# Optimization experiments

Measured on AMD Instinct MI355X. Metric: run time of the kernel, lower is better.

Reference implementation:

```python
import jax, jax.numpy as jnp
import numpy as np

SCALE = 1.0 / (64 ** 0.5)  # 1/sqrt(dim_key)

def setup_inputs() -> dict:
    key = jax.random.key(0)
    ks = jax.random.split(key, 8)
    B, S, D, H, dk = 4, 2048, 1024, 16, 64
    s = 0.02
    return {
        "values": jax.random.normal(ks[0], (B, S, D), jnp.float32),
        "queries": jax.random.normal(ks[1], (B, S, D), jnp.float32),
        "keys": jax.random.normal(ks[2], (B, S, D), jnp.float32),
        "Wq": jax.random.normal(ks[3], (H, D, dk), jnp.float32) * s,
        "bq": jnp.zeros((H, dk), jnp.float32),
        "Wk": jax.random.normal(ks[4], (H, D, dk), jnp.float32) * s,
        "bk": jnp.zeros((H, dk), jnp.float32),
        "Wv": jax.random.normal(ks[5], (H, D, dk), jnp.float32) * s,
        "bv": jnp.zeros((H, dk), jnp.float32),
        "Wo": jax.random.normal(ks[6], (D, D), jnp.float32) * s,
        "bo": jnp.zeros((D,), jnp.float32),
    }

def reference(values, queries, keys, Wq, bq, Wk, bk, Wv, bv, Wo, bo):
    # Per-head projections, batched across heads: [B,S,D] x [H,D,dk] -> [B,H,S,dk]
    q = jnp.einsum('bsd,hdk->bhsk', queries, Wq) + bq[None, :, None, :]
    k = jnp.einsum('bsd,hdk->bhsk', keys, Wk) + bk[None, :, None, :]
    v = jnp.einsum('bsd,hdk->bhsk', values, Wv) + bv[None, :, None, :]
    # Scaled dot-product scores [B,H,S,S]
    scores = jnp.einsum('bhqk,bhsk->bhqs', q, k) * SCALE
    S = scores.shape[-1]
    causal = jnp.tril(jnp.ones((S, S), bool))
    scores = jnp.where(causal, scores, jnp.float32(-1e19))
    attn = jax.nn.softmax(scores, axis=-1)
    ctx = jnp.einsum('bhqs,bhsk->bhqk', attn, v)  # [B,H,S,dk]
    # Concat heads along last axis (head-major, matching tf.concat order)
    B, H, Sq, dk = ctx.shape
    ctx = jnp.transpose(ctx, (0, 2, 1, 3)).reshape(B, Sq, H * dk)
    return ctx @ Wo + bo
```

## Files before the change

### kernel.cpp

```cpp
#include <hip/hip_runtime.h>
#include <hip/hip_bf16.h>
#include <cstdint>

#define B_ 4
#define H_ 16
#define S_ 2048
#define D_ 1024
#define DK 64
#define QSCALE 0.18033688f

typedef float f32x4 __attribute__((ext_vector_type(4)));
typedef short bf8 __attribute__((ext_vector_type(8)));
typedef unsigned short u16;

__device__ __forceinline__ u16 f2bf(float x){
  union { float f; uint32_t u; } c; c.f = x;
  uint32_t u = c.u;
  uint32_t r = (u + 0x7FFFu + ((u >> 16) & 1u)) >> 16;
  return (u16)r;
}

__device__ __forceinline__ uint32_t pk2bf(float a, float b){
  __hip_bfloat162 t = __float22bfloat162_rn(make_float2(a, b));
  uint32_t r; __builtin_memcpy(&r, &t, 4); return r;
}

__device__ __forceinline__ void gl16(const void* g, void* l){
  __builtin_amdgcn_global_load_lds(
      (const __attribute__((address_space(1))) void*)g,
      (__attribute__((address_space(3))) void*)l, 16, 0, 0);
}

__global__ __launch_bounds__(256) void cvt_in(
    const float* __restrict__ q, const float* __restrict__ k,
    const float* __restrict__ v, u16* __restrict__ o)
{
  const size_t N8 = (size_t)1 << 20;
  const size_t tot = 3 * N8;
  const size_t step = (size_t)gridDim.x * 256;
  for (size_t g0 = (size_t)blockIdx.x*256 + threadIdx.x; g0 < tot; g0 += step){
    int t = (int)(g0 >> 20);
    size_t r = g0 & (N8 - 1);
    const float* src = (t==0 ? q : (t==1 ? k : v));
    const float4* s4 = reinterpret_cast<const float4*>(src + r*8);
    float4 a = s4[0], b = s4[1];
    uint4 w;
    w.x = pk2bf(a.x,a.y); w.y = pk2bf(a.z,a.w);
    w.z = pk2bf(b.x,b.y); w.w = pk2bf(b.z,b.w);
    *reinterpret_cast<uint4*>(o + ((size_t)t << 23) + r*8) = w;
  }
}

__global__ __launch_bounds__(256) void wtrans3(
    const float* __restrict__ Wq, const float* __restrict__ Wk,
    const float* __restrict__ Wv, u16* __restrict__ oq,
    u16* __restrict__ ok, u16* __restrict__ ov)
{
  __shared__ u16 T[64*72];
  const int tid = threadIdx.x;
  const int z = blockIdx.z, t = z >> 4, hh = z & 15;
  const float* src = (t==0 ? Wq : t==1 ? Wk : Wv) + (size_t)hh * (D_*DK);
  u16* dst = (t==0 ? oq : t==1 ? ok : ov) + (size_t)hh * (DK*D_);
  const int r0 = blockIdx.y*64;
  #pragma unroll
  for (int p=0;p<4;++p){
    int r  = p*16 + (tid>>4);
    int c4 = (tid&15)*4;
    float4 v = *reinterpret_cast<const float4*>(&src[(size_t)(r0+r)*DK + c4]);
    uint2 w; w.x = pk2bf(v.x, v.y); w.y = pk2bf(v.z, v.w);
    *reinterpret_cast<uint2*>(&T[r*72 + c4]) = w;
  }
  __syncthreads();
  const int c = tid>>2, rg = (tid&3)*16;
  u16 tmp[16];
  #pragma unroll
  for (int i=0;i<16;++i) tmp[i] = T[(rg+i)*72 + c];
  *reinterpret_cast<bf8*>(&dst[(size_t)c*D_ + r0 + rg])     = *reinterpret_cast<bf8*>(&tmp[0]);
  *reinterpret_cast<bf8*>(&dst[(size_t)c*D_ + r0 + rg + 8]) = *reinterpret_cast<bf8*>(&tmp[8]);
}

__global__ __launch_bounds__(256) void wtrans(
    const float* __restrict__ in, u16* __restrict__ out, int R, int C)
{
  __shared__ u16 T[64*72];
  const int tid = threadIdx.x;
  const int r0 = blockIdx.y*64, c0 = blockIdx.x*64;
  #pragma unroll
  for (int p=0;p<4;++p){
    int r  = p*16 + (tid>>4);
    int c4 = (tid&15)*4;
    float4 v = *reinterpret_cast<const float4*>(&in[(size_t)(r0+r)*C + c0 + c4]);
    uint2 w; w.x = pk2bf(v.x, v.y); w.y = pk2bf(v.z, v.w);
    *reinterpret_cast<uint2*>(&T[r*72 + c4]) = w;
  }
  __syncthreads();
  const int c = tid>>2, rg = (tid&3)*16;
  u16 tmp[16];
  #pragma unroll
  for (int i=0;i<16;++i) tmp[i] = T[(rg+i)*72 + c];
  *reinterpret_cast<bf8*>(&out[(size_t)(c0+c)*R + r0 + rg])     = *reinterpret_cast<bf8*>(&tmp[0]);
  *reinterpret_cast<bf8*>(&out[(size_t)(c0+c)*R + r0 + rg + 8]) = *reinterpret_cast<bf8*>(&tmp[8]);
}

__global__ __launch_bounds__(256) void gemm_qkv(
    const u16* __restrict__ Ab,
    const u16* __restrict__ Bq, const u16* __restrict__ Bk,
    const u16* __restrict__ Bv,
    const float* __restrict__ bq, const float* __restrict__ bk,
    const float* __restrict__ bv,
    u16* __restrict__ oq, u16* __restrict__ ok, u16* __restrict__ ov)
{
  __shared__ u16 As[2][128*64];
  __shared__ u16 Bs[2][128*64];
  const int tid = threadIdx.x;
  const int wid = tid>>6, lane = tid&63, g = lane>>4, l15 = lane&15;
  const int z = blockIdx.x >> 9, bid = blockIdx.x & 511;
  const u16* A     = Ab + ((size_t)z << 23);
  const u16*   Bt  = (z==0 ? Bq : z==1 ? Bk : Bv);
  const float* bias= (z==0 ? bq : z==1 ? bk : bv);
  u16* Out         = (z==0 ? oq : z==1 ? ok : ov);
  const float osc  = (z==0 ? QSCALE : 1.0f);
  const int xcd = bid & 7, i = bid >> 3;
  const int cb = i & 7, rb = xcd*8 + (i>>3);
  const int row0 = rb*128, col0 = cb*128;
  const int wr = wid>>1, wc = wid&1;

  f32x4 acc[4][4];
  #pragma unroll
  for (int m=0;m<4;++m)
    #pragma unroll
    for (int n=0;n<4;++n) acc[m][n] = (f32x4){0.f,0.f,0.f,0.f};

  auto STAGE = [&](int buf, int k0){
    #pragma unroll
    for (int p=0;p<4;++p){
      int r0l = wid*32 + p*8;
      int row = r0l + (lane>>3);
      int ch = (lane&7) ^ (row&7);
      gl16(A  + (size_t)(row0+row)*D_ + k0 + ch*8, &As[buf][r0l*64]);
      gl16(Bt + (size_t)(col0+row)*D_ + k0 + ch*8, &Bs[buf][r0l*64]);
    }
  };

  int cur = 0;
  STAGE(0, 0);
  asm volatile("s_waitcnt vmcnt(0)" ::: "memory");
  __syncthreads();

  for (int k0 = 0; k0 < D_; k0 += 64) {
    if (k0 + 64 < D_) STAGE(cur^1, k0 + 64);

    bf8 af[4][2], bfm[4][2];
    #pragma unroll
    for (int m=0;m<4;++m){
      int row = wr*64 + m*16 + l15;
      af[m][0] = *reinterpret_cast<const bf8*>(&As[cur][row*64 + ((g     ^(row&7))*8)]);
      af[m][1] = *reinterpret_cast<const bf8*>(&As[cur][row*64 + (((4+g) ^(row&7))*8)]);
    }
    #pragma unroll
    for (int n=0;n<4;++n){
      int row = wc*64 + n*16 + l15;
      bfm[n][0] = *reinterpret_cast<const bf8*>(&Bs[cur][row*64 + ((g     ^(row&7))*8)]);
      bfm[n][1] = *reinterpret_cast<const bf8*>(&Bs[cur][row*64 + (((4+g) ^(row&7))*8)]);
    }
    #pragma unroll
    for (int m=0;m<4;++m)
      #pragma unroll
      for (int n=0;n<4;++n){
        acc[m][n] = __builtin_amdgcn_mfma_f32_16x16x32_bf16(af[m][0], bfm[n][0], acc[m][n], 0,0,0);
        acc[m][n] = __builtin_amdgcn_mfma_f32_16x16x32_bf16(af[m][1], bfm[n][1], acc[m][n], 0,0,0);
      }
    asm volatile("s_waitcnt vmcnt(0)" ::: "memory");
    __syncthreads();
    cur ^= 1;
  }

  #pragma unroll
  for (int m=0;m<4;++m){
    #pragma unroll
    for (int n=0;n<4;++n){
      int col = col0 + wc*64 + n*16 + l15;
      float bs = bias[col];
      if (z == 2){
        int rowb = row0 + wr*64 + m*16 + g*4;
        int b = rowb>>11, s = rowb&2047;
        int h = col>>6, dkk = col&63;
        ushort4 pk;
        pk.x = f2bf(acc[m][n][0]+bs); pk.y = f2bf(acc[m][n][1]+bs);
        pk.z = f2bf(acc[m][n][2]+bs); pk.w = f2bf(acc[m][n][3]+bs);
        *reinterpret_cast<ushort4*>(&Out[(((size_t)(b*H_+h)*DK)+dkk)*S_ + s]) = pk;
      } else {
        #pragma unroll
        for (int r=0;r<4;++r){
          int row = row0 + wr*64 + m*16 + g*4 + r;
          float v = (acc[m][n][r] + bs)*osc;
          int b = row>>11, s = row&2047;
          int h = col>>6, dkk = col&63;
          Out[(((size_t)(b*H_+h)*S_)+s)*DK + dkk] = f2bf(v);
        }
      }
    }
  }
}

__global__ __launch_bounds__(256) void gemm_out(
    const u16* __restrict__ A, const u16* __restrict__ Bt,
    const float* __restrict__ bias, float* __restrict__ Outp)
{
  __shared__ u16 As[2][128*64];
  __shared__ u16 Bs[2][128*64];
  const int tid = threadIdx.x;
  const int wid = tid>>6, lane = tid&63, g = lane>>4, l15 = lane&15;
  const int bid = blockIdx.x;
  const int xcd = bid & 7, i = bid >> 3;
  const int cb = i & 7, rb = xcd*8 + (i>>3);
  const int row0 = rb*128, col0 = cb*128;
  const int wr = wid>>1, wc = wid&1;

  f32x4 acc[4][4];
  #pragma unroll
  for (int m=0;m<4;++m)
    #pragma unroll
    for (int n=0;n<4;++n) acc[m][n] = (f32x4){0.f,0.f,0.f,0.f};

  auto STAGE = [&](int buf, int k0){
    #pragma unroll
    for (int p=0;p<4;++p){
      int r0l = wid*32 + p*8;
      int row = r0l + (lane>>3);
      int ch = (lane&7) ^ (row&7);
      gl16(A  + (size_t)(row0+row)*D_ + k0 + ch*8, &As[buf][r0l*64]);
      gl16(Bt + (size_t)(col0+row)*D_ + k0 + ch*8, &Bs[buf][r0l*64]);
    }
  };

  int cur = 0;
  STAGE(0, 0);
  asm volatile("s_waitcnt vmcnt(0)" ::: "memory");
  __syncthreads();

  for (int k0 = 0; k0 < D_; k0 += 64) {
    if (k0 + 64 < D_) STAGE(cur^1, k0 + 64);

    bf8 af[4][2], bfm[4][2];
    #pragma unroll
    for (int m=0;m<4;++m){
      int row = wr*64 + m*16 + l15;
      af[m][0] = *reinterpret_cast<const bf8*>(&As[cur][row*64 + ((g     ^(row&7))*8)]);
      af[m][1] = *reinterpret_cast<const bf8*>(&As[cur][row*64 + (((4+g) ^(row&7))*8)]);
    }
    #pragma unroll
    for (int n=0;n<4;++n){
      int row = wc*64 + n*16 + l15;
      bfm[n][0] = *reinterpret_cast<const bf8*>(&Bs[cur][row*64 + ((g     ^(row&7))*8)]);
      bfm[n][1] = *reinterpret_cast<const bf8*>(&Bs[cur][row*64 + (((4+g) ^(row&7))*8)]);
    }
    #pragma unroll
    for (int m=0;m<4;++m)
      #pragma unroll
      for (int n=0;n<4;++n){
        acc[m][n] = __builtin_amdgcn_mfma_f32_16x16x32_bf16(af[m][0], bfm[n][0], acc[m][n], 0,0,0);
        acc[m][n] = __builtin_amdgcn_mfma_f32_16x16x32_bf16(af[m][1], bfm[n][1], acc[m][n], 0,0,0);
      }
    asm volatile("s_waitcnt vmcnt(0)" ::: "memory");
    __syncthreads();
    cur ^= 1;
  }

  #pragma unroll
  for (int m=0;m<4;++m){
    #pragma unroll
    for (int n=0;n<4;++n){
      int col = col0 + wc*64 + n*16 + l15;
      float bs = bias[col];
      #pragma unroll
      for (int r=0;r<4;++r){
        int row = row0 + wr*64 + m*16 + g*4 + r;
        Outp[(size_t)row*D_ + col] = acc[m][n][r] + bs;
      }
    }
  }
}

__global__ __launch_bounds__(256) void attn_kernel(
    const u16* __restrict__ qp, const u16* __restrict__ kp,
    const u16* __restrict__ vt, u16* __restrict__ ctx)
{
  __shared__ u16 Kl[2][64*64];
  __shared__ u16 Vl[2][64*64];
  __shared__ u16 Pl[4][32*72];
  const int tid = threadIdx.x;
  const int wid = tid>>6, lane = tid&63, g = lane>>4, l15 = lane&15;
  const int bid0 = blockIdx.x;
  const int xx = bid0 & 7, yy = bid0 >> 3;
  const int bh = xx + 8*(yy >> 3);
  const int jj = yy & 7;
  const int b = bh >> 4, h = bh & 15;
  const size_t base = (size_t)bh * S_ * DK;

  bf8 ones;
  #pragma unroll
  for (int i=0;i<8;++i) ones[i] = (short)0x3F80;

  const int qts[2] = { jj, 15-jj };

  #pragma unroll 1
  for (int qi=0; qi<2; ++qi){
    const int qt = qts[qi];
    const int Q0 = qt*128;
    bf8 aq[2][2];
    #pragma unroll
    for (int qs=0;qs<2;++qs){
      int qrow = Q0 + wid*32 + qs*16 + l15;
      aq[qs][0] = *reinterpret_cast<const bf8*>(&qp[base + (size_t)qrow*DK +      g*8]);
      aq[qs][1] = *reinterpret_cast<const bf8*>(&qp[base + (size_t)qrow*DK + 32 + g*8]);
    }

    f32x4 acco[2][4], acc_l[2];
    #pragma unroll
    for (int qs=0;qs<2;++qs){
      #pragma unroll
      for (int nd=0;nd<4;++nd) acco[qs][nd] = (f32x4){0.f,0.f,0.f,0.f};
      acc_l[qs] = (f32x4){0.f,0.f,0.f,0.f};
    }

    auto STAGE = [&](int buf, int kt){
      const int k0 = kt*64;
      #pragma unroll
      for (int p=0;p<2;++p){
        int r0l = wid*16 + p*8;
        int row = r0l + (lane>>3);
        int ch  = (lane&7) ^ (row&7);
        gl16(kp + base + (size_t)(k0+row)*DK + ch*8, &Kl[buf][r0l*64]);
        gl16(vt + base + (size_t)row*S_ + k0 + ch*8, &Vl[buf][r0l*64]);
      }
    };

    const int nk = 2*qt + 2;
    int cur = 0;
    STAGE(cur, 0);
    asm volatile("s_waitcnt vmcnt(0)" ::: "memory");
    __syncthreads();

    for (int kt = 0; kt < nk; ++kt){
      if (kt < nk-1) STAGE(cur^1, kt+1);

      f32x4 sc[2][4];
      #pragma unroll
      for (int n=0;n<4;++n){
        int row = n*16 + l15;
        bf8 b0 = *reinterpret_cast<const bf8*>(&Kl[cur][row*64 + ((g     ^(row&7))*8)]);
        bf8 b1 = *reinterpret_cast<const bf8*>(&Kl[cur][row*64 + (((4+g) ^(row&7))*8)]);
        #pragma unroll
        for (int qs=0;qs<2;++qs){
          f32x4 z = (f32x4){0.f,0.f,0.f,0.f};
          z = __builtin_amdgcn_mfma_f32_16x16x32_bf16(aq[qs][0], b0, z, 0,0,0);
          z = __builtin_amdgcn_mfma_f32_16x16x32_bf16(aq[qs][1], b1, z, 0,0,0);
          sc[qs][n] = z;
        }
      }
      if (kt >= nk-2){
        const int k0 = kt*64;
        #pragma unroll
        for (int qs=0;qs<2;++qs){
          #pragma unroll
          for (int n=0;n<4;++n){
            #pragma unroll
            for (int r=0;r<4;++r){
              int qg = Q0 + wid*32 + qs*16 + g*4 + r;
              int kg = k0 + n*16 + l15;
              if (kg > qg) sc[qs][n][r] = -1e30f;
            }
          }
        }
      }
      #pragma unroll
      for (int qs=0;qs<2;++qs){
        #pragma unroll
        for (int n=0;n<4;++n){
          #pragma unroll
          for (int r=0;r<4;++r){
            float p = __builtin_amdgcn_exp2f(sc[qs][n][r]);
            union { float f; uint32_t u; } cu; cu.f = p;
            Pl[wid][(qs*16 + g*4 + r)*72 + n*16 + l15] = (u16)(cu.u >> 16);
          }
        }
      }
      asm volatile("s_waitcnt lgkmcnt(0)" ::: "memory");
      __builtin_amdgcn_sched_barrier(0);

      bf8 pa[2][2];
      #pragma unroll
      for (int qs=0;qs<2;++qs){
        pa[qs][0] = *reinterpret_cast<const bf8*>(&Pl[wid][(qs*16 + l15)*72 +      g*8]);
        pa[qs][1] = *reinterpret_cast<const bf8*>(&Pl[wid][(qs*16 + l15)*72 + 32 + g*8]);
        acc_l[qs] = __builtin_amdgcn_mfma_f32_16x16x32_bf16(pa[qs][0], ones, acc_l[qs], 0,0,0);
        acc_l[qs] = __builtin_amdgcn_mfma_f32_16x16x32_bf16(pa[qs][1], ones, acc_l[qs], 0,0,0);
      }
      #pragma unroll
      for (int nd=0;nd<4;++nd){
        int row = nd*16 + l15;
        bf8 v0 = *reinterpret_cast<const bf8*>(&Vl[cur][row*64 + ((g     ^(row&7))*8)]);
        bf8 v1 = *reinterpret_cast<const bf8*>(&Vl[cur][row*64 + (((4+g) ^(row&7))*8)]);
        #pragma unroll
        for (int qs=0;qs<2;++qs){
          acco[qs][nd] = __builtin_amdgcn_mfma_f32_16x16x32_bf16(pa[qs][0], v0, acco[qs][nd], 0,0,0);
          acco[qs][nd] = __builtin_amdgcn_mfma_f32_16x16x32_bf16(pa[qs][1], v1, acco[qs][nd], 0,0,0);
        }
      }
      asm volatile("s_waitcnt vmcnt(0)" ::: "memory");
      __syncthreads();
      cur ^= 1;
    }

    #pragma unroll
    for (int qs=0;qs<2;++qs){
      float rl[4];
      #pragma unroll
      for (int r=0;r<4;++r) rl[r] = __builtin_amdgcn_rcpf(acc_l[qs][r]);
      #pragma unroll
      for (int nd=0;nd<4;++nd){
        #pragma unroll
        for (int r=0;r<4;++r){
          int qg = Q0 + wid*32 + qs*16 + g*4 + r;
          float v = acco[qs][nd][r] * rl[r];
          ctx[((size_t)(b*S_) + qg)*D_ + h*DK + nd*16 + l15] = f2bf(v);
        }
      }
    }
  }
}

extern "C" void kernel_launch(void* const* d_in, const int* in_sizes, int n_in,
                              void* d_out, int out_size, void* d_ws, size_t ws_size,
                              hipStream_t stream)
{
  const float* values  = (const float*)d_in[0];
  const float* queries = (const float*)d_in[1];
  const float* keys    = (const float*)d_in[2];
  const float* Wq = (const float*)d_in[3];
  const float* bq = (const float*)d_in[4];
  const float* Wk = (const float*)d_in[5];
  const float* bk = (const float*)d_in[6];
  const float* Wv = (const float*)d_in[7];
  const float* bv = (const float*)d_in[8];
  const float* Wo = (const float*)d_in[9];
  const float* bo = (const float*)d_in[10];
  float* out = (float*)d_out;

  const size_t NE = (size_t)B_*H_*S_*DK;
  const size_t WE = (size_t)D_*D_;
  u16* cvt = (u16*)d_ws;
  u16* qp  = cvt + 3*NE;
  u16* kp  = qp + NE;
  u16* vtb = kp + NE;
  u16* wtq = vtb + NE;
  u16* wtk = wtq + WE;
  u16* wtv = wtk + WE;
  u16* wto = wtv + WE;
  u16* ctx = cvt;

  cvt_in<<<3072, 256, 0, stream>>>(queries, keys, values, cvt);
  wtrans3<<<dim3(1,16,48), 256, 0, stream>>>(Wq, Wk, Wv, wtq, wtk, wtv);
  wtrans<<<dim3(16,16,1), 256, 0, stream>>>(Wo, wto, D_, D_);
  gemm_qkv<<<1536, 256, 0, stream>>>(cvt, wtq, wtk, wtv,
                                     bq, bk, bv, qp, kp, vtb);
  attn_kernel<<<512, 256, 0, stream>>>(qp, kp, vtb, ctx);
  gemm_out<<<512, 256, 0, stream>>>(ctx, wto, bo, out);
}
```

Baseline: 186.5 us.

## Use 128x256 GEMM tiles with 8 waves and split attention query tiles

Merges the QKV and output-projection GEMMs into one templated kernel that uses 512 threads and 128x256 tiles. It splits each k-step into two half-phases separated by barriers and raises wave priority around the MFMA blocks to interleave LDS reads with matrix math. The attention kernel now gives each block a single query tile (1024 blocks) instead of a balanced pair of tiles, ordered heaviest-first. This trades the old per-block load balancing for more parallelism and a longest-first schedule, and the larger GEMM tiles use more registers and LDS per block.

```diff
diff --git a/kernel.cpp b/kernel.cpp
--- a/kernel.cpp
+++ b/kernel.cpp
@@ -102,28 +102,31 @@
   *reinterpret_cast<bf8*>(&out[(size_t)(c0+c)*R + r0 + rg + 8]) = *reinterpret_cast<bf8*>(&tmp[8]);
 }
 
-__global__ __launch_bounds__(256) void gemm_qkv(
+template<int ISOUT>
+__global__ __launch_bounds__(512, 2) void gemm256(
     const u16* __restrict__ Ab,
-    const u16* __restrict__ Bq, const u16* __restrict__ Bk,
-    const u16* __restrict__ Bv,
-    const float* __restrict__ bq, const float* __restrict__ bk,
-    const float* __restrict__ bv,
-    u16* __restrict__ oq, u16* __restrict__ ok, u16* __restrict__ ov)
+    const u16* __restrict__ B0, const u16* __restrict__ B1,
+    const u16* __restrict__ B2,
+    const float* __restrict__ c0, const float* __restrict__ c1,
+    const float* __restrict__ c2,
+    u16* __restrict__ o0, u16* __restrict__ o1, u16* __restrict__ o2,
+    float* __restrict__ ofp)
 {
   __shared__ u16 As[2][128*64];
-  __shared__ u16 Bs[2][128*64];
+  __shared__ u16 Bs[2][256*64];
   const int tid = threadIdx.x;
   const int wid = tid>>6, lane = tid&63, g = lane>>4, l15 = lane&15;
-  const int z = blockIdx.x >> 9, bid = blockIdx.x & 511;
-  const u16* A     = Ab + ((size_t)z << 23);
-  const u16*   Bt  = (z==0 ? Bq : z==1 ? Bk : Bv);
-  const float* bias= (z==0 ? bq : z==1 ? bk : bv);
-  u16* Out         = (z==0 ? oq : z==1 ? ok : ov);
+  const int z   = ISOUT ? 0 : (blockIdx.x >> 8);
+  const int bid = ISOUT ? blockIdx.x : (blockIdx.x & 255);
+  const u16* A     = ISOUT ? Ab : Ab + ((size_t)z << 23);
+  const u16* Bt    = ISOUT ? B0 : (z==0 ? B0 : z==1 ? B1 : B2);
+  const float* bias= ISOUT ? c0 : (z==0 ? c0 : z==1 ? c1 : c2);
+  u16* Out         = (z==0 ? o0 : z==1 ? o1 : o2);
   const float osc  = (z==0 ? QSCALE : 1.0f);
-  const int xcd = bid & 7, i = bid >> 3;
-  const int cb = i & 7, rb = xcd*8 + (i>>3);
-  const int row0 = rb*128, col0 = cb*128;
-  const int wr = wid>>1, wc = wid&1;
+  const int xcd = bid & 7, idx = bid >> 3;
+  const int mb = xcd*8 + (idx>>2), nb = idx&3;
+  const int row0 = mb*128, col0 = nb*256;
+  const int wr = wid>>2, wc = wid&3;
 
   f32x4 acc[4][4];
   #pragma unroll
@@ -133,11 +136,17 @@
 
   auto STAGE = [&](int buf, int k0){
     #pragma unroll
-    for (int p=0;p<4;++p){
-      int r0l = wid*32 + p*8;
+    for (int i=0;i<2;++i){
+      int r0l = wid*16 + i*8;
       int row = r0l + (lane>>3);
-      int ch = (lane&7) ^ (row&7);
-      gl16(A  + (size_t)(row0+row)*D_ + k0 + ch*8, &As[buf][r0l*64]);
+      int ch  = (lane&7) ^ (row&7);
+      gl16(A + (size_t)(row0+row)*D_ + k0 + ch*8, &As[buf][r0l*64]);
+    }
+    #pragma unroll
+    for (int i=0;i<4;++i){
+      int r0l = wid*32 + i*8;
+      int row = r0l + (lane>>3);
+      int ch  = (lane&7) ^ (row&7);
       gl16(Bt + (size_t)(col0+row)*D_ + k0 + ch*8, &Bs[buf][r0l*64]);
     }
   };
@@ -145,33 +154,57 @@
   int cur = 0;
   STAGE(0, 0);
   asm volatile("s_waitcnt vmcnt(0)" ::: "memory");
-  __syncthreads();
+  asm volatile("s_barrier" ::: "memory");
 
   for (int k0 = 0; k0 < D_; k0 += 64) {
     if (k0 + 64 < D_) STAGE(cur^1, k0 + 64);
 
-    bf8 af[4][2], bfm[4][2];
-    #pragma unroll
-    for (int m=0;m<4;++m){
-      int row = wr*64 + m*16 + l15;
-      af[m][0] = *reinterpret_cast<const bf8*>(&As[cur][row*64 + ((g     ^(row&7))*8)]);
-      af[m][1] = *reinterpret_cast<const bf8*>(&As[cur][row*64 + (((4+g) ^(row&7))*8)]);
-    }
+    bf8 bfm[4][2];
     #pragma unroll
     for (int n=0;n<4;++n){
       int row = wc*64 + n*16 + l15;
       bfm[n][0] = *reinterpret_cast<const bf8*>(&Bs[cur][row*64 + ((g     ^(row&7))*8)]);
       bfm[n][1] = *reinterpret_cast<const bf8*>(&Bs[cur][row*64 + (((4+g) ^(row&7))*8)]);
     }
-    #pragma unroll
-    for (int m=0;m<4;++m)
+    bf8 af0[2][2];
+    #pragma unroll
+    for (int m=0;m<2;++m){
+      int row = wr*64 + m*16 + l15;
+      af0[m][0] = *reinterpret_cast<const bf8*>(&As[cur][row*64 + ((g     ^(row&7))*8)]);
+      af0[m][1] = *reinterpret_cast<const bf8*>(&As[cur][row*64 + (((4+g) ^(row&7))*8)]);
+    }
+    asm volatile("s_barrier" ::: "memory");
+    __builtin_amdgcn_s_setprio(1);
+    #pragma unroll
+    for (int m=0;m<2;++m)
       #pragma unroll
       for (int n=0;n<4;++n){
-        acc[m][n] = __builtin_amdgcn_mfma_f32_16x16x32_bf16(af[m][0], bfm[n][0], acc[m][n], 0,0,0);
-        acc[m][n] = __builtin_amdgcn_mfma_f32_16x16x32_bf16(af[m][1], bfm[n][1], acc[m][n], 0,0,0);
-      }
+        acc[m][n] = __builtin_amdgcn_mfma_f32_16x16x32_bf16(af0[m][0], bfm[n][0], acc[m][n], 0,0,0);
+        acc[m][n] = __builtin_amdgcn_mfma_f32_16x16x32_bf16(af0[m][1], bfm[n][1], acc[m][n], 0,0,0);
+      }
+    __builtin_amdgcn_s_setprio(0);
+    __builtin_amdgcn_sched_barrier(0);
+    asm volatile("s_barrier" ::: "memory");
+    bf8 af1[2][2];
+    #pragma unroll
+    for (int m=0;m<2;++m){
+      int row = wr*64 + (m+2)*16 + l15;
+      af1[m][0] = *reinterpret_cast<const bf8*>(&As[cur][row*64 + ((g     ^(row&7))*8)]);
+      af1[m][1] = *reinterpret_cast<const bf8*>(&As[cur][row*64 + (((4+g) ^(row&7))*8)]);
+    }
+    asm volatile("s_barrier" ::: "memory");
+    __builtin_amdgcn_s_setprio(1);
+    #pragma unroll
+    for (int m=0;m<2;++m)
+      #pragma unroll
+      for (int n=0;n<4;++n){
+        acc[m+2][n] = __builtin_amdgcn_mfma_f32_16x16x32_bf16(af1[m][0], bfm[n][0], acc[m+2][n], 0,0,0);
+        acc[m+2][n] = __builtin_amdgcn_mfma_f32_16x16x32_bf16(af1[m][1], bfm[n][1], acc[m+2][n], 0,0,0);
+      }
+    __builtin_amdgcn_s_setprio(0);
+    __builtin_amdgcn_sched_barrier(0);
     asm volatile("s_waitcnt vmcnt(0)" ::: "memory");
-    __syncthreads();
+    asm volatile("s_barrier" ::: "memory");
     cur ^= 1;
   }
 
@@ -181,7 +214,13 @@
     for (int n=0;n<4;++n){
       int col = col0 + wc*64 + n*16 + l15;
       float bs = bias[col];
-      if (z == 2){
+      if (ISOUT){
+        #pragma unroll
+        for (int r=0;r<4;++r){
+          int row = row0 + wr*64 + m*16 + g*4 + r;
+          ofp[(size_t)row*D_ + col] = acc[m][n][r] + bs;
+        }
+      } else if (z == 2){
         int rowb = row0 + wr*64 + m*16 + g*4;
         int b = rowb>>11, s = rowb&2047;
         int h = col>>6, dkk = col&63;
@@ -203,85 +242,6 @@
   }
 }
 
-__global__ __launch_bounds__(256) void gemm_out(
-    const u16* __restrict__ A, const u16* __restrict__ Bt,
-    const float* __restrict__ bias, float* __restrict__ Outp)
-{
-  __shared__ u16 As[2][128*64];
-  __shared__ u16 Bs[2][128*64];
-  const int tid = threadIdx.x;
-  const int wid = tid>>6, lane = tid&63, g = lane>>4, l15 = lane&15;
-  const int bid = blockIdx.x;
-  const int xcd = bid & 7, i = bid >> 3;
-  const int cb = i & 7, rb = xcd*8 + (i>>3);
-  const int row0 = rb*128, col0 = cb*128;
-  const int wr = wid>>1, wc = wid&1;
-
-  f32x4 acc[4][4];
-  #pragma unroll
-  for (int m=0;m<4;++m)
-    #pragma unroll
-    for (int n=0;n<4;++n) acc[m][n] = (f32x4){0.f,0.f,0.f,0.f};
-
-  auto STAGE = [&](int buf, int k0){
-    #pragma unroll
-    for (int p=0;p<4;++p){
-      int r0l = wid*32 + p*8;
-      int row = r0l + (lane>>3);
-      int ch = (lane&7) ^ (row&7);
-      gl16(A  + (size_t)(row0+row)*D_ + k0 + ch*8, &As[buf][r0l*64]);
-      gl16(Bt + (size_t)(col0+row)*D_ + k0 + ch*8, &Bs[buf][r0l*64]);
-    }
-  };
-
-  int cur = 0;
-  STAGE(0, 0);
-  asm volatile("s_waitcnt vmcnt(0)" ::: "memory");
-  __syncthreads();
-
-  for (int k0 = 0; k0 < D_; k0 += 64) {
-    if (k0 + 64 < D_) STAGE(cur^1, k0 + 64);
-
-    bf8 af[4][2], bfm[4][2];
-    #pragma unroll
-    for (int m=0;m<4;++m){
-      int row = wr*64 + m*16 + l15;
-      af[m][0] = *reinterpret_cast<const bf8*>(&As[cur][row*64 + ((g     ^(row&7))*8)]);
-      af[m][1] = *reinterpret_cast<const bf8*>(&As[cur][row*64 + (((4+g) ^(row&7))*8)]);
-    }
-    #pragma unroll
-    for (int n=0;n<4;++n){
-      int row = wc*64 + n*16 + l15;
-      bfm[n][0] = *reinterpret_cast<const bf8*>(&Bs[cur][row*64 + ((g     ^(row&7))*8)]);
-      bfm[n][1] = *reinterpret_cast<const bf8*>(&Bs[cur][row*64 + (((4+g) ^(row&7))*8)]);
-    }
-    #pragma unroll
-    for (int m=0;m<4;++m)
-      #pragma unroll
-      for (int n=0;n<4;++n){
-        acc[m][n] = __builtin_amdgcn_mfma_f32_16x16x32_bf16(af[m][0], bfm[n][0], acc[m][n], 0,0,0);
-        acc[m][n] = __builtin_amdgcn_mfma_f32_16x16x32_bf16(af[m][1], bfm[n][1], acc[m][n], 0,0,0);
-      }
-    asm volatile("s_waitcnt vmcnt(0)" ::: "memory");
-    __syncthreads();
-    cur ^= 1;
-  }
-
-  #pragma unroll
-  for (int m=0;m<4;++m){
-    #pragma unroll
-    for (int n=0;n<4;++n){
-      int col = col0 + wc*64 + n*16 + l15;
-      float bs = bias[col];
-      #pragma unroll
-      for (int r=0;r<4;++r){
-        int row = row0 + wr*64 + m*16 + g*4 + r;
-        Outp[(size_t)row*D_ + col] = acc[m][n][r] + bs;
-      }
-    }
-  }
-}
-
 __global__ __launch_bounds__(256) void attn_kernel(
     const u16* __restrict__ qp, const u16* __restrict__ kp,
     const u16* __restrict__ vt, u16* __restrict__ ctx)
@@ -293,8 +253,8 @@
   const int wid = tid>>6, lane = tid&63, g = lane>>4, l15 = lane&15;
   const int bid0 = blockIdx.x;
   const int xx = bid0 & 7, yy = bid0 >> 3;
-  const int bh = xx + 8*(yy >> 3);
-  const int jj = yy & 7;
+  const int bh = xx + 8*(yy & 7);
+  const int qt = 15 - (yy >> 3);
   const int b = bh >> 4, h = bh & 15;
   const size_t base = (size_t)bh * S_ * DK;
 
@@ -302,130 +262,124 @@
   #pragma unroll
   for (int i=0;i<8;++i) ones[i] = (short)0x3F80;
 
-  const int qts[2] = { jj, 15-jj };
-
-  #pragma unroll 1
-  for (int qi=0; qi<2; ++qi){
-    const int qt = qts[qi];
-    const int Q0 = qt*128;
-    bf8 aq[2][2];
-    #pragma unroll
-    for (int qs=0;qs<2;++qs){
-      int qrow = Q0 + wid*32 + qs*16 + l15;
-      aq[qs][0] = *reinterpret_cast<const bf8*>(&qp[base + (size_t)qrow*DK +      g*8]);
-      aq[qs][1] = *reinterpret_cast<const bf8*>(&qp[base + (size_t)qrow*DK + 32 + g*8]);
-    }
-
-    f32x4 acco[2][4], acc_l[2];
-    #pragma unroll
-    for (int qs=0;qs<2;++qs){
-      #pragma unroll
-      for (int nd=0;nd<4;++nd) acco[qs][nd] = (f32x4){0.f,0.f,0.f,0.f};
-      acc_l[qs] = (f32x4){0.f,0.f,0.f,0.f};
-    }
-
-    auto STAGE = [&](int buf, int kt){
+  const int Q0 = qt*128;
+  bf8 aq[2][2];
+  #pragma unroll
+  for (int qs=0;qs<2;++qs){
+    int qrow = Q0 + wid*32 + qs*16 + l15;
+    aq[qs][0] = *reinterpret_cast<const bf8*>(&qp[base + (size_t)qrow*DK +      g*8]);
+    aq[qs][1] = *reinterpret_cast<const bf8*>(&qp[base + (size_t)qrow*DK + 32 + g*8]);
+  }
+
+  f32x4 acco[2][4], acc_l[2];
+  #pragma unroll
+  for (int qs=0;qs<2;++qs){
+    #pragma unroll
+    for (int nd=0;nd<4;++nd) acco[qs][nd] = (f32x4){0.f,0.f,0.f,0.f};
+    acc_l[qs] = (f32x4){0.f,0.f,0.f,0.f};
+  }
+
+  auto STAGE = [&](int buf, int kt){
+    const int k0 = kt*64;
+    #pragma unroll
+    for (int p=0;p<2;++p){
+      int r0l = wid*16 + p*8;
+      int row = r0l + (lane>>3);
+      int ch  = (lane&7) ^ (row&7);
+      gl16(kp + base + (size_t)(k0+row)*DK + ch*8, &Kl[buf][r0l*64]);
+      gl16(vt + base + (size_t)row*S_ + k0 + ch*8, &Vl[buf][r0l*64]);
+    }
+  };
+
+  const int nk = 2*qt + 2;
+  int cur = 0;
+  STAGE(cur, 0);
+  asm volatile("s_waitcnt vmcnt(0)" ::: "memory");
+  __syncthreads();
+
+  for (int kt = 0; kt < nk; ++kt){
+    if (kt < nk-1) STAGE(cur^1, kt+1);
+
+    f32x4 sc[2][4];
+    #pragma unroll
+    for (int n=0;n<4;++n){
+      int row = n*16 + l15;
+      bf8 b0 = *reinterpret_cast<const bf8*>(&Kl[cur][row*64 + ((g     ^(row&7))*8)]);
+      bf8 b1 = *reinterpret_cast<const bf8*>(&Kl[cur][row*64 + (((4+g) ^(row&7))*8)]);
+      #pragma unroll
+      for (int qs=0;qs<2;++qs){
+        f32x4 z = (f32x4){0.f,0.f,0.f,0.f};
+        z = __builtin_amdgcn_mfma_f32_16x16x32_bf16(aq[qs][0], b0, z, 0,0,0);
+        z = __builtin_amdgcn_mfma_f32_16x16x32_bf16(aq[qs][1], b1, z, 0,0,0);
+        sc[qs][n] = z;
+      }
+    }
+    if (kt >= nk-2){
       const int k0 = kt*64;
-      #pragma unroll
-      for (int p=0;p<2;++p){
-        int r0l = wid*16 + p*8;
-        int row = r0l + (lane>>3);
-        int ch  = (lane&7) ^ (row&7);
-        gl16(kp + base + (size_t)(k0+row)*DK + ch*8, &Kl[buf][r0l*64]);
-        gl16(vt + base + (size_t)row*S_ + k0 + ch*8, &Vl[buf][r0l*64]);
-      }
-    };
-
-    const int nk = 2*qt + 2;
-    int cur = 0;
-    STAGE(cur, 0);
-    asm volatile("s_waitcnt vmcnt(0)" ::: "memory");
-    __syncthreads();
-
-    for (int kt = 0; kt < nk; ++kt){
-      if (kt < nk-1) STAGE(cur^1, kt+1);
-
-      f32x4 sc[2][4];
-      #pragma unroll
-      for (int n=0;n<4;++n){
-        int row = n*16 + l15;
-        bf8 b0 = *reinterpret_cast<const bf8*>(&Kl[cur][row*64 + ((g     ^(row&7))*8)]);
-        bf8 b1 = *reinterpret_cast<const bf8*>(&Kl[cur][row*64 + (((4+g) ^(row&7))*8)]);
-        #pragma unroll
-        for (int qs=0;qs<2;++qs){
-          f32x4 z = (f32x4){0.f,0.f,0.f,0.f};
-          z = __builtin_amdgcn_mfma_f32_16x16x32_bf16(aq[qs][0], b0, z, 0,0,0);
-          z = __builtin_amdgcn_mfma_f32_16x16x32_bf16(aq[qs][1], b1, z, 0,0,0);
-          sc[qs][n] = z;
-        }
-      }
-      if (kt >= nk-2){
-        const int k0 = kt*64;
-        #pragma unroll
-        for (int qs=0;qs<2;++qs){
-          #pragma unroll
-          for (int n=0;n<4;++n){
-            #pragma unroll
-            for (int r=0;r<4;++r){
-              int qg = Q0 + wid*32 + qs*16 + g*4 + r;
-              int kg = k0 + n*16 + l15;
-              if (kg > qg) sc[qs][n][r] = -1e30f;
-            }
-          }
-        }
-      }
       #pragma unroll
       for (int qs=0;qs<2;++qs){
         #pragma unroll
         for (int n=0;n<4;++n){
           #pragma unroll
           for (int r=0;r<4;++r){
-            float p = __builtin_amdgcn_exp2f(sc[qs][n][r]);
-            union { float f; uint32_t u; } cu; cu.f = p;
-            Pl[wid][(qs*16 + g*4 + r)*72 + n*16 + l15] = (u16)(cu.u >> 16);
+            int qg = Q0 + wid*32 + qs*16 + g*4 + r;
+            int kg = k0 + n*16 + l15;
+            if (kg > qg) sc[qs][n][r] = -1e30f;
           }
         }
       }
-      asm volatile("s_waitcnt lgkmcnt(0)" ::: "memory");
-      __builtin_amdgcn_sched_barrier(0);
-
-      bf8 pa[2][2];
-      #pragma unroll
-      for (int qs=0;qs<2;++qs){
-        pa[qs][0] = *reinterpret_cast<const bf8*>(&Pl[wid][(qs*16 + l15)*72 +      g*8]);
-        pa[qs][1] = *reinterpret_cast<const bf8*>(&Pl[wid][(qs*16 + l15)*72 + 32 + g*8]);
-        acc_l[qs] = __builtin_amdgcn_mfma_f32_16x16x32_bf16(pa[qs][0], ones, acc_l[qs], 0,0,0);
-        acc_l[qs] = __builtin_amdgcn_mfma_f32_16x16x32_bf16(pa[qs][1], ones, acc_l[qs], 0,0,0);
-      }
-      #pragma unroll
-      for (int nd=0;nd<4;++nd){
-        int row = nd*16 + l15;
-        bf8 v0 = *reinterpret_cast<const bf8*>(&Vl[cur][row*64 + ((g     ^(row&7))*8)]);
-        bf8 v1 = *reinterpret_cast<const bf8*>(&Vl[cur][row*64 + (((4+g) ^(row&7))*8)]);
-        #pragma unroll
-        for (int qs=0;qs<2;++qs){
-          acco[qs][nd] = __builtin_amdgcn_mfma_f32_16x16x32_bf16(pa[qs][0], v0, acco[qs][nd], 0,0,0);
-          acco[qs][nd] = __builtin_amdgcn_mfma_f32_16x16x32_bf16(pa[qs][1], v1, acco[qs][nd], 0,0,0);
-        }
-      }
-      asm volatile("s_waitcnt vmcnt(0)" ::: "memory");
-      __syncthreads();
-      cur ^= 1;
-    }
-
+    }
     #pragma unroll
     for (int qs=0;qs<2;++qs){
-      float rl[4];
-      #pragma unroll
-      for (int r=0;r<4;++r) rl[r] = __builtin_amdgcn_rcpf(acc_l[qs][r]);
-      #pragma unroll
-      for (int nd=0;nd<4;++nd){
+      #pragma unroll
+      for (int n=0;n<4;++n){
         #pragma unroll
         for (int r=0;r<4;++r){
-          int qg = Q0 + wid*32 + qs*16 + g*4 + r;
-          float v = acco[qs][nd][r] * rl[r];
-          ctx[((size_t)(b*S_) + qg)*D_ + h*DK + nd*16 + l15] = f2bf(v);
+          float p = __builtin_amdgcn_exp2f(sc[qs][n][r]);
+          union { float f; uint32_t u; } cu; cu.f = p;
+          Pl[wid][(qs*16 + g*4 + r)*72 + n*16 + l15] = (u16)(cu.u >> 16);
         }
+      }
+    }
+    asm volatile("s_waitcnt lgkmcnt(0)" ::: "memory");
+    __builtin_amdgcn_sched_barrier(0);
+
+    bf8 pa[2][2];
+    #pragma unroll
+    for (int qs=0;qs<2;++qs){
+      pa[qs][0] = *reinterpret_cast<const bf8*>(&Pl[wid][(qs*16 + l15)*72 +      g*8]);
+      pa[qs][1] = *reinterpret_cast<const bf8*>(&Pl[wid][(qs*16 + l15)*72 + 32 + g*8]);
+      acc_l[qs] = __builtin_amdgcn_mfma_f32_16x16x32_bf16(pa[qs][0], ones, acc_l[qs], 0,0,0);
+      acc_l[qs] = __builtin_amdgcn_mfma_f32_16x16x32_bf16(pa[qs][1], ones, acc_l[qs], 0,0,0);
+    }
+    #pragma unroll
+    for (int nd=0;nd<4;++nd){
+      int row = nd*16 + l15;
+      bf8 v0 = *reinterpret_cast<const bf8*>(&Vl[cur][row*64 + ((g     ^(row&7))*8)]);
+      bf8 v1 = *reinterpret_cast<const bf8*>(&Vl[cur][row*64 + (((4+g) ^(row&7))*8)]);
+      #pragma unroll
+      for (int qs=0;qs<2;++qs){
+        acco[qs][nd] = __builtin_amdgcn_mfma_f32_16x16x32_bf16(pa[qs][0], v0, acco[qs][nd], 0,0,0);
+        acco[qs][nd] = __builtin_amdgcn_mfma_f32_16x16x32_bf16(pa[qs][1], v1, acco[qs][nd], 0,0,0);
+      }
+    }
+    asm volatile("s_waitcnt vmcnt(0)" ::: "memory");
+    __syncthreads();
+    cur ^= 1;
+  }
+
+  #pragma unroll
+  for (int qs=0;qs<2;++qs){
+    float rl[4];
+    #pragma unroll
+    for (int r=0;r<4;++r) rl[r] = __builtin_amdgcn_rcpf(acc_l[qs][r]);
+    #pragma unroll
+    for (int nd=0;nd<4;++nd){
+      #pragma unroll
+      for (int r=0;r<4;++r){
+        int qg = Q0 + wid*32 + qs*16 + g*4 + r;
+        float v = acco[qs][nd][r] * rl[r];
+        ctx[((size_t)(b*S_) + qg)*D_ + h*DK + nd*16 + l15] = f2bf(v);
       }
     }
   }
@@ -463,8 +417,9 @@
   cvt_in<<<3072, 256, 0, stream>>>(queries, keys, values, cvt);
   wtrans3<<<dim3(1,16,48), 256, 0, stream>>>(Wq, Wk, Wv, wtq, wtk, wtv);
   wtrans<<<dim3(16,16,1), 256, 0, stream>>>(Wo, wto, D_, D_);
-  gemm_qkv<<<1536, 256, 0, stream>>>(cvt, wtq, wtk, wtv,
-                                     bq, bk, bv, qp, kp, vtb);
-  attn_kernel<<<512, 256, 0, stream>>>(qp, kp, vtb, ctx);
-  gemm_out<<<512, 256, 0, stream>>>(ctx, wto, bo, out);
-}
+  gemm256<0><<<768, 512, 0, stream>>>(cvt, wtq, wtk, wtv,
+                                      bq, bk, bv, qp, kp, vtb, nullptr);
+  attn_kernel<<<1024, 256, 0, stream>>>(qp, kp, vtb, ctx);
+  gemm256<1><<<256, 512, 0, stream>>>(ctx, wto, nullptr, nullptr,
+                                      bo, nullptr, nullptr, qp, nullptr, nullptr, out);
+}
```

Result: slower. 197.9 us (+6.1%).
